# Optimization experiments

Hardware: AMD Instinct MI355X
Metric: run time of the kernel (lower is better)

The kernel has to match this reference:

```python
import jax, jax.numpy as jnp
import numpy as np

SLOPE = 25.0  # snntorch fast_sigmoid default surrogate slope

@jax.custom_vjp
def spike(u):
    return (u > 0).astype(u.dtype)

def _spike_fwd(u):
    return spike(u), u

def _spike_bwd(u, g):
    return (g / (1.0 + SLOPE * jnp.abs(u)) ** 2,)

spike.defvjp(_spike_fwd, _spike_bwd)

def fake_quant(W):
    # brevitas-style int8 per-tensor symmetric fake-quant with STE
    s = jnp.max(jnp.abs(W)) / 127.0
    q = jnp.clip(jnp.round(W / s), -127.0, 127.0) * s
    return W + jax.lax.stop_gradient(q - W)

def setup_inputs() -> dict:
    key = jax.random.key(0)
    ks = jax.random.split(key, 8)
    B, NIN, T = 256, 512, 256
    H1, H2, OUT = 512, 512, 128
    data = jax.random.normal(ks[0], (B, NIN, T), dtype=jnp.float32)
    W1 = jax.random.normal(ks[1], (H1, NIN), dtype=jnp.float32) / np.sqrt(NIN)
    W2 = jax.random.normal(ks[2], (H2, H1), dtype=jnp.float32) / np.sqrt(H1)
    Wrec = jax.random.normal(ks[3], (H2, H2), dtype=jnp.float32) / np.sqrt(H2)
    W3 = jax.random.normal(ks[4], (OUT, H2), dtype=jnp.float32) / np.sqrt(H2)
    beta = jnp.float32(0.9)
    th = jnp.float32(1.0)
    return {"data": data, "W1": W1, "W2": W2, "Wrec": Wrec, "W3": W3,
            "beta1": beta, "th1": th, "beta_r": beta, "th_r": th,
            "beta2": beta, "th2": th}

def reference(data, W1, W2, Wrec, W3, beta1, th1, beta_r, th_r, beta2, th2):
    B = data.shape[0]
    H1, H2, OUT = W1.shape[0], W2.shape[0], W3.shape[0]
    W1q = fake_quant(W1)
    W2q = fake_quant(W2)
    Wrq = fake_quant(Wrec)
    W3q = fake_quant(W3)
    b1 = jnp.clip(beta1, 0.0, 1.0)
    br = jnp.clip(beta_r, 0.0, 1.0)
    b2 = jnp.clip(beta2, 0.0, 1.0)
    # time-major input: [T, B, NIN]
    xs = jnp.transpose(data, (2, 0, 1))

    def step(carry, x):
        m1, mr, sr, m2 = carry
        # leaky1: reset zero, reset_delay=False
        m1 = b1 * m1 + x @ W1q.T
        s1 = spike(m1 - th1)
        m1 = m1 * (1.0 - s1)
        # recurrent LIF (RLeaky-like), reset zero, reset_delay=True:
        # previous spike resets the membrane at the start of this step
        h = s1 @ W2q.T + sr @ Wrq.T
        mr = (br * mr + h) * (1.0 - sr)
        sr = spike(mr - th_r)
        # leaky2: reset zero, reset_delay=False
        m2 = b2 * m2 + sr @ W3q.T
        s2 = spike(m2 - th2)
        m2 = m2 * (1.0 - s2)
        return (m1, mr, sr, m2), s2

    init = (jnp.zeros((B, H1), jnp.float32),
            jnp.zeros((B, H2), jnp.float32),
            jnp.zeros((B, H2), jnp.float32),
            jnp.zeros((B, OUT), jnp.float32))
    _, spk_rec = jax.lax.scan(step, init, xs)
    return spk_rec  # [T, B, OUT]
```

## Files before the change

### kernel.cpp

```cpp
#include <hip/hip_runtime.h>

#define B_   256
#define NIN_ 512
#define T_   256
#define H1_  512
#define H2_  512
#define OUT_ 128

typedef __attribute__((ext_vector_type(4))) int i32x4;
typedef __attribute__((address_space(1))) const unsigned int* gl_cu;
typedef __attribute__((address_space(3))) unsigned int* ls_u;

__global__ void absmax_k(const float* __restrict__ W1, const float* __restrict__ W2,
                         const float* __restrict__ Wr, const float* __restrict__ W3,
                         float* __restrict__ scales) {
  const float* W; int n;
  switch (blockIdx.x) {
    case 0:  W = W1; n = H1_ * NIN_; break;
    case 1:  W = W2; n = H2_ * H1_;  break;
    case 2:  W = Wr; n = H2_ * H2_;  break;
    default: W = W3; n = OUT_ * H2_; break;
  }
  int tid = threadIdx.x;
  float m = 0.f;
  const float4* W4 = (const float4*)W;
  int n4 = n >> 2;
  for (int i = tid; i < n4; i += 256) {
    float4 v = W4[i];
    m = fmaxf(m, fmaxf(fmaxf(fabsf(v.x), fabsf(v.y)), fmaxf(fabsf(v.z), fabsf(v.w))));
  }
  __shared__ float red[256];
  red[tid] = m;
  __syncthreads();
  for (int s = 128; s > 0; s >>= 1) {
    if (tid < s) red[tid] = fmaxf(red[tid], red[tid + s]);
    __syncthreads();
  }
  if (tid == 0) scales[blockIdx.x] = red[0] / 127.0f;
}

__global__ void quant_all_k(const float* __restrict__ W1, const float* __restrict__ W2,
                            const float* __restrict__ Wr, const float* __restrict__ W3,
                            const float* __restrict__ scales,
                            float* __restrict__ W1qT, signed char* __restrict__ W2i8,
                            signed char* __restrict__ WrT, signed char* __restrict__ W3i8) {
  const int blk = blockIdx.x;
  if (blk < 1024) {
    int idx = blk * 256 + threadIdx.x;
    int h = idx & (H1_ - 1), i = idx >> 9;
    float s = scales[0];
    float q = rintf(W1[h * NIN_ + i] / s);
    q = fminf(fmaxf(q, -127.f), 127.f);
    W1qT[idx] = q * s;
  } else if (blk < 2048) {
    int idx = (blk - 1024) * 256 + threadIdx.x;
    float s = scales[1];
    float q = rintf(W2[idx] / s);
    q = fminf(fmaxf(q, -127.f), 127.f);
    W2i8[idx] = (signed char)q;
  } else if (blk < 3072) {
    int idx = (blk - 2048) * 256 + threadIdx.x;
    int r = idx >> 9, c = idx & (H2_ - 1);
    float s = scales[2];
    float q = rintf(Wr[idx] / s);
    q = fminf(fmaxf(q, -127.f), 127.f);
    WrT[(size_t)c * H2_ + r] = (signed char)q;
  } else {
    int idx = (blk - 3072) * 256 + threadIdx.x;
    float s = scales[3];
    float q = rintf(W3[idx] / s);
    q = fminf(fmaxf(q, -127.f), 127.f);
    W3i8[idx] = (signed char)q;
  }
}

__global__ __launch_bounds__(512, 6) void gemm_cur1_k(const float* __restrict__ data,
                                                      const float* __restrict__ W1qT,
                                                      float* __restrict__ cur1) {
  const int b  = blockIdx.y;
  const int t0 = (blockIdx.x >> 2) << 7;
  const int h0 = (blockIdx.x & 3) << 7;
  const int tid = threadIdx.x;

  __shared__ float As[2][16][128];
  __shared__ float Bs[2][16][128];

  const int ty = tid >> 4, tx = tid & 15;
  const int wv = tid >> 6;
  const int ln = tid & 63;

  float acc[4][8];
#pragma unroll
  for (int i = 0; i < 4; i++)
#pragma unroll
    for (int j = 0; j < 8; j++) acc[i][j] = 0.f;

  const float* dbase = data + (size_t)b * NIN_ * T_;

  auto issue = [&](int kb, int buf) {
    const int kr = (wv << 1) + (ln >> 5);
    const float* ga = dbase + (size_t)(kb + kr) * T_ + t0 + ((ln & 31) << 2);
    __builtin_amdgcn_global_load_lds((gl_cu)ga, (ls_u)&As[buf][wv << 1][0], 16, 0, 0);
    const float* gb = W1qT + (size_t)(kb + kr) * H1_ + h0 + ((ln & 31) << 2);
    __builtin_amdgcn_global_load_lds((gl_cu)gb, (ls_u)&Bs[buf][wv << 1][0], 16, 0, 0);
  };

  issue(0, 0);

  for (int p = 0; p < 32; p++) {
    const int cur = p & 1;
    __syncthreads();
    if (p < 31) issue((p + 1) << 4, cur ^ 1);
#pragma unroll
    for (int k = 0; k < 16; k++) {
      float4 A0 = *(const float4*)&As[cur][k][ty * 4];
      float4 B0 = *(const float4*)&Bs[cur][k][tx * 4];
      float4 B1 = *(const float4*)&Bs[cur][k][64 + tx * 4];
      float a[4] = {A0.x, A0.y, A0.z, A0.w};
      float w[8] = {B0.x, B0.y, B0.z, B0.w, B1.x, B1.y, B1.z, B1.w};
#pragma unroll
      for (int i = 0; i < 4; i++)
#pragma unroll
        for (int j = 0; j < 8; j++)
          acc[i][j] = fmaf(a[i], w[j], acc[i][j]);
    }
  }

#pragma unroll
  for (int i = 0; i < 4; i++) {
    int row = ty * 4 + i;
    float* op = cur1 + (size_t)(t0 + row) * (B_ * H1_) + (size_t)b * H1_ + h0;
    float4 cA = {acc[i][0], acc[i][1], acc[i][2], acc[i][3]};
    float4 cB = {acc[i][4], acc[i][5], acc[i][6], acc[i][7]};
    *(float4*)(op + tx * 4)      = cA;
    *(float4*)(op + 64 + tx * 4) = cB;
  }
}

__global__ __launch_bounds__(256) void scan1_k(const float* __restrict__ cur1,
                                               unsigned char* __restrict__ s1u,
                                               const float* __restrict__ beta1p,
                                               const float* __restrict__ th1p) {
  const int n0 = (blockIdx.x * 256 + threadIdx.x) << 2;
  const float b1 = fminf(fmaxf(beta1p[0], 0.f), 1.f);
  const float th1 = th1p[0];
  const size_t S = (size_t)B_ * H1_;
  float m0 = 0.f, m1 = 0.f, m2 = 0.f, m3 = 0.f;
#pragma unroll 2
  for (int t = 0; t < T_; t++) {
    float4 c = *(const float4*)(cur1 + (size_t)t * S + n0);
    uchar4 o;
    m0 = b1 * m0 + c.x; bool s0 = m0 - th1 > 0.f; if (s0) m0 = 0.f; o.x = s0;
    m1 = b1 * m1 + c.y; bool s1 = m1 - th1 > 0.f; if (s1) m1 = 0.f; o.y = s1;
    m2 = b1 * m2 + c.z; bool s2 = m2 - th1 > 0.f; if (s2) m2 = 0.f; o.z = s2;
    m3 = b1 * m3 + c.w; bool s3 = m3 - th1 > 0.f; if (s3) m3 = 0.f; o.w = s3;
    *(uchar4*)(s1u + (size_t)t * S + n0) = o;
  }
}

__global__ __launch_bounds__(256) void gemm_spk_k(const unsigned char* __restrict__ A8,
                                                  const signed char* __restrict__ Bw,
                                                  float* __restrict__ C, int N) {
  __shared__ __align__(16) signed char As[128 * 80];
  __shared__ __align__(16) signed char Bs[128 * 80];
  const int tid = threadIdx.x;
  const int m0 = blockIdx.y << 7;
  const int n0 = blockIdx.x << 7;
  const int lane = tid & 63, wave = tid >> 6;
  const int quad = lane >> 4, lm = lane & 15;
  const int wm = wave << 5;

  i32x4 acc[2][8];
#pragma unroll
  for (int s = 0; s < 2; s++)
#pragma unroll
    for (int n = 0; n < 8; n++) acc[s][n] = (i32x4){0, 0, 0, 0};

  const int row = tid >> 2;
  const int offB = (tid & 3) << 4;

  for (int kb = 0; kb < 512; kb += 64) {
    uint4 av[2], bv[2];
#pragma unroll
    for (int i = 0; i < 2; i++) {
      const int r = row + (i << 6);
      av[i] = *(const uint4*)(A8 + (size_t)(m0 + r) * 512 + kb + offB);
      bv[i] = *(const uint4*)(Bw + (size_t)(n0 + r) * 512 + kb + offB);
    }
    __syncthreads();
#pragma unroll
    for (int i = 0; i < 2; i++) {
      const int r = row + (i << 6);
      *(uint4*)&As[r * 80 + offB] = av[i];
      *(uint4*)&Bs[r * 80 + offB] = bv[i];
    }
    __syncthreads();
    i32x4 a0 = *(const i32x4*)&As[(wm + lm) * 80 + (quad << 4)];
    i32x4 a1 = *(const i32x4*)&As[(wm + 16 + lm) * 80 + (quad << 4)];
    i32x4 bq[8];
#pragma unroll
    for (int n = 0; n < 8; n++)
      bq[n] = *(const i32x4*)&Bs[((n << 4) + lm) * 80 + (quad << 4)];
#pragma unroll
    for (int n = 0; n < 8; n++) {
      acc[0][n] = __builtin_amdgcn_mfma_i32_16x16x64_i8(a0, bq[n], acc[0][n], 0, 0, 0);
      acc[1][n] = __builtin_amdgcn_mfma_i32_16x16x64_i8(a1, bq[n], acc[1][n], 0, 0, 0);
    }
    __syncthreads();
  }

#pragma unroll
  for (int s = 0; s < 2; s++)
#pragma unroll
    for (int n = 0; n < 8; n++) {
      int orow = m0 + wm + (s << 4) + quad * 4;
      int col = n0 + (n << 4) + lm;
#pragma unroll
      for (int r = 0; r < 4; r++)
        C[(size_t)(orow + r) * N + col] = (float)acc[s][n][r];
    }
}

__device__ __forceinline__ void unp_add(unsigned w, int* a) {
  int iw = (int)w;
  a[0] += (iw << 24) >> 24;
  a[1] += (iw << 16) >> 24;
  a[2] += (iw << 8) >> 24;
  a[3] += iw >> 24;
}

__global__ __launch_bounds__(1024) void recurrent_k(
    const float* __restrict__ cur2a,
    const signed char* __restrict__ WrT,
    unsigned char* __restrict__ sru,
    const float* __restrict__ scales,
    const float* __restrict__ betarp, const float* __restrict__ thrp) {
  const int b = blockIdx.x;
  const int tid = threadIdx.x;
  const float s2sc = scales[1];
  const float srsc = scales[2];
  const float br = fminf(fmaxf(betarp[0], 0.f), 1.f);
  const float thr = thrp[0];

  const unsigned* WrT4 = (const unsigned*)WrT;

  __shared__ unsigned WrL[256 * 128];
  __shared__ int red[8][H2_];
  __shared__ int lstLo[2][256];
  __shared__ int lstHi[2][256];
  __shared__ int ncLo[2], ncHi[2];

  {
    const uint4* src = (const uint4*)WrT4;
    uint4* dst = (uint4*)WrL;
    for (int i = tid; i < 8192; i += 1024) dst[i] = src[i];
  }
  if (tid < 2) { ncLo[tid] = 0; ncHi[tid] = 0; }
  __syncthreads();

  float mr = 0.f, sr_own = 0.f;
  const int g = tid >> 7;
  const int c = tid & 127;

  for (int t = 0; t < T_; t++) {
    const int old = t & 1, nxt = old ^ 1;
    float c2 = 0.f;
    if (tid < H2_) c2 = cur2a[((size_t)t * B_ + b) * H2_ + tid];
    if (tid == 1022) ncLo[nxt] = 0;
    if (tid == 1023) ncHi[nxt] = 0;
    const int nLo = ncLo[old];
    const int nHi = ncHi[old];
    const int* LLo = lstLo[old];
    const int* LHi = lstHi[old];

    int a4[4] = {0, 0, 0, 0};
    {
      int k = g;
      for (; k + 56 < nLo; k += 64) {
        int i0 = LLo[k],      i1 = LLo[k + 8],  i2 = LLo[k + 16], i3 = LLo[k + 24];
        int i4 = LLo[k + 32], i5 = LLo[k + 40], i6 = LLo[k + 48], i7 = LLo[k + 56];
        unsigned w0 = WrL[(i0 << 7) + c], w1 = WrL[(i1 << 7) + c];
        unsigned w2 = WrL[(i2 << 7) + c], w3 = WrL[(i3 << 7) + c];
        unsigned w4 = WrL[(i4 << 7) + c], w5 = WrL[(i5 << 7) + c];
        unsigned w6 = WrL[(i6 << 7) + c], w7 = WrL[(i7 << 7) + c];
        unp_add(w0, a4); unp_add(w1, a4); unp_add(w2, a4); unp_add(w3, a4);
        unp_add(w4, a4); unp_add(w5, a4); unp_add(w6, a4); unp_add(w7, a4);
      }
      for (; k + 24 < nLo; k += 32) {
        int i0 = LLo[k], i1 = LLo[k + 8], i2 = LLo[k + 16], i3 = LLo[k + 24];
        unsigned w0 = WrL[(i0 << 7) + c], w1 = WrL[(i1 << 7) + c];
        unsigned w2 = WrL[(i2 << 7) + c], w3 = WrL[(i3 << 7) + c];
        unp_add(w0, a4); unp_add(w1, a4); unp_add(w2, a4); unp_add(w3, a4);
      }
      for (; k < nLo; k += 8) unp_add(WrL[(LLo[k] << 7) + c], a4);
    }
    {
      int k = g;
      for (; k + 56 < nHi; k += 64) {
        int i0 = LHi[k],      i1 = LHi[k + 8],  i2 = LHi[k + 16], i3 = LHi[k + 24];
        int i4 = LHi[k + 32], i5 = LHi[k + 40], i6 = LHi[k + 48], i7 = LHi[k + 56];
        unsigned w0 = WrT4[(i0 << 7) + c], w1 = WrT4[(i1 << 7) + c];
        unsigned w2 = WrT4[(i2 << 7) + c], w3 = WrT4[(i3 << 7) + c];
        unsigned w4 = WrT4[(i4 << 7) + c], w5 = WrT4[(i5 << 7) + c];
        unsigned w6 = WrT4[(i6 << 7) + c], w7 = WrT4[(i7 << 7) + c];
        unp_add(w0, a4); unp_add(w1, a4); unp_add(w2, a4); unp_add(w3, a4);
        unp_add(w4, a4); unp_add(w5, a4); unp_add(w6, a4); unp_add(w7, a4);
      }
      for (; k + 24 < nHi; k += 32) {
        int i0 = LHi[k], i1 = LHi[k + 8], i2 = LHi[k + 16], i3 = LHi[k + 24];
        unsigned w0 = WrT4[(i0 << 7) + c], w1 = WrT4[(i1 << 7) + c];
        unsigned w2 = WrT4[(i2 << 7) + c], w3 = WrT4[(i3 << 7) + c];
        unp_add(w0, a4); unp_add(w1, a4); unp_add(w2, a4); unp_add(w3, a4);
      }
      for (; k < nHi; k += 8) unp_add(WrT4[(LHi[k] << 7) + c], a4);
    }
    *(int4*)&red[g][c << 2] = make_int4(a4[0], a4[1], a4[2], a4[3]);
    __syncthreads();

    bool spike = false;
    if (tid < H2_) {
      int acc = red[0][tid] + red[1][tid] + red[2][tid] + red[3][tid]
              + red[4][tid] + red[5][tid] + red[6][tid] + red[7][tid];
      float h = s2sc * c2 + srsc * (float)acc;
      mr = (br * mr + h) * (1.f - sr_own);
      sr_own = (mr - thr > 0.f) ? 1.f : 0.f;
      sru[((size_t)t * B_ + b) * H2_ + tid] = (unsigned char)(sr_own != 0.f);
      spike = (sr_own != 0.f);
    }
    unsigned long long bm = __ballot(spike);
    if (bm != 0ull) {
      const int lane = tid & 63;
      const int ldr = (int)__ffsll((long long)bm) - 1;
      int* cnt = (tid < 256) ? &ncLo[nxt] : &ncHi[nxt];
      int* dst = (tid < 256) ? lstLo[nxt] : lstHi[nxt];
      int base = 0;
      if (lane == ldr) base = atomicAdd(cnt, (int)__popcll(bm));
      base = __shfl(base, ldr);
      if (spike)
        dst[base + (int)__popcll(bm & ((1ull << lane) - 1ull))] = tid;
    }
    __syncthreads();
  }
}

__global__ __launch_bounds__(256) void scan3_k(const float* __restrict__ cur3,
                                               float* __restrict__ out,
                                               const float* __restrict__ scales,
                                               const float* __restrict__ beta2p,
                                               const float* __restrict__ th2p) {
  const int n = blockIdx.x * 256 + threadIdx.x;
  const float s3sc = scales[3];
  const float b2 = fminf(fmaxf(beta2p[0], 0.f), 1.f);
  const float th2 = th2p[0];
  const size_t S = (size_t)B_ * OUT_;
  float m2 = 0.f;
  for (int t = 0; t < T_; t += 4) {
    float v0 = cur3[(size_t)t * S + n];
    float v1 = cur3[(size_t)(t + 1) * S + n];
    float v2 = cur3[(size_t)(t + 2) * S + n];
    float v3 = cur3[(size_t)(t + 3) * S + n];
    m2 = b2 * m2 + s3sc * v0; float p0 = (m2 - th2 > 0.f) ? 1.f : 0.f; m2 *= (1.f - p0);
    out[(size_t)t * S + n] = p0;
    m2 = b2 * m2 + s3sc * v1; float p1 = (m2 - th2 > 0.f) ? 1.f : 0.f; m2 *= (1.f - p1);
    out[(size_t)(t + 1) * S + n] = p1;
    m2 = b2 * m2 + s3sc * v2; float p2 = (m2 - th2 > 0.f) ? 1.f : 0.f; m2 *= (1.f - p2);
    out[(size_t)(t + 2) * S + n] = p2;
    m2 = b2 * m2 + s3sc * v3; float p3 = (m2 - th2 > 0.f) ? 1.f : 0.f; m2 *= (1.f - p3);
    out[(size_t)(t + 3) * S + n] = p3;
  }
}

extern "C" void kernel_launch(void* const* d_in, const int* in_sizes, int n_in,
                              void* d_out, int out_size, void* d_ws, size_t ws_size,
                              hipStream_t stream) {
  const float* data  = (const float*)d_in[0];
  const float* W1    = (const float*)d_in[1];
  const float* W2    = (const float*)d_in[2];
  const float* Wr    = (const float*)d_in[3];
  const float* W3    = (const float*)d_in[4];
  const float* beta1 = (const float*)d_in[5];
  const float* th1   = (const float*)d_in[6];
  const float* betar = (const float*)d_in[7];
  const float* thr   = (const float*)d_in[8];
  const float* beta2 = (const float*)d_in[9];
  const float* th2   = (const float*)d_in[10];

  char* ws = (char*)d_ws;
  float*         scales = (float*)ws;
  float*         W1qT   = (float*)(ws + 4096);
  signed char*   W2i8   = (signed char*)(ws + 4096 + 1048576);
  signed char*   W3i8   = (signed char*)(ws + 4096 + 1048576 + 524288);
  signed char*   WrT    = (signed char*)(ws + 4096 + 1048576 + 524288 + 131072);
  float*         regA   = (float*)(ws + (size_t)4194304);
  unsigned char* regB   = (unsigned char*)(ws + (size_t)4194304 + 134217728);

  float* cur1  = regA;
  float* cur2a = regA;
  float* cur3  = regA;
  unsigned char* s1u = regB;
  unsigned char* sru = regB + (size_t)33554432;

  hipLaunchKernelGGL(absmax_k, dim3(4), dim3(256), 0, stream, W1, W2, Wr, W3, scales);
  hipLaunchKernelGGL(quant_all_k, dim3(3328), dim3(256), 0, stream,
                     W1, W2, Wr, W3, scales, W1qT, W2i8, WrT, W3i8);

  hipLaunchKernelGGL(gemm_cur1_k, dim3(8, 256), dim3(512), 0, stream, data, W1qT, cur1);
  hipLaunchKernelGGL(scan1_k, dim3((B_ * H1_) / 1024), dim3(256), 0, stream, cur1, s1u, beta1, th1);
  hipLaunchKernelGGL(gemm_spk_k, dim3(4, 512), dim3(256), 0, stream, s1u, W2i8, cur2a, H2_);
  hipLaunchKernelGGL(recurrent_k, dim3(256), dim3(1024), 0, stream, cur2a, WrT, sru, scales, betar, thr);
  hipLaunchKernelGGL(gemm_spk_k, dim3(1, 512), dim3(256), 0, stream, sru, W3i8, cur3, OUT_);
  hipLaunchKernelGGL(scan3_k, dim3((B_ * OUT_) / 256), dim3(256), 0, stream, cur3, (float*)d_out, scales, beta2, th2);
}
```

Measured before the change: 1.083 ms.

## Double-buffer LDS in spike GEMM and widen scan1 parallelism to one neuron per thread

The spike GEMM now keeps two LDS buffers and issues the next K-tile's global loads before the current tile's MFMAs. This overlaps memory latency with compute and drops one barrier per iteration. The first scan kernel changes from four neurons per thread to one, launching four times as many blocks for more memory-level parallelism. The catch is scalar byte stores and 4-byte loads in place of vectorized float4/uchar4 accesses, plus twice the LDS per GEMM block, which may lower occupancy.

Result: faster. 1.035 ms (-4.4%).

```diff
diff --git a/kernel.cpp b/kernel.cpp
--- a/kernel.cpp
+++ b/kernel.cpp
@@ -141,28 +141,32 @@
                                                unsigned char* __restrict__ s1u,
                                                const float* __restrict__ beta1p,
                                                const float* __restrict__ th1p) {
-  const int n0 = (blockIdx.x * 256 + threadIdx.x) << 2;
+  const int n = blockIdx.x * 256 + threadIdx.x;
   const float b1 = fminf(fmaxf(beta1p[0], 0.f), 1.f);
   const float th1 = th1p[0];
   const size_t S = (size_t)B_ * H1_;
-  float m0 = 0.f, m1 = 0.f, m2 = 0.f, m3 = 0.f;
-#pragma unroll 2
-  for (int t = 0; t < T_; t++) {
-    float4 c = *(const float4*)(cur1 + (size_t)t * S + n0);
-    uchar4 o;
-    m0 = b1 * m0 + c.x; bool s0 = m0 - th1 > 0.f; if (s0) m0 = 0.f; o.x = s0;
-    m1 = b1 * m1 + c.y; bool s1 = m1 - th1 > 0.f; if (s1) m1 = 0.f; o.y = s1;
-    m2 = b1 * m2 + c.z; bool s2 = m2 - th1 > 0.f; if (s2) m2 = 0.f; o.z = s2;
-    m3 = b1 * m3 + c.w; bool s3 = m3 - th1 > 0.f; if (s3) m3 = 0.f; o.w = s3;
-    *(uchar4*)(s1u + (size_t)t * S + n0) = o;
+  float m1 = 0.f;
+  for (int t = 0; t < T_; t += 4) {
+    float c0 = cur1[(size_t)t * S + n];
+    float c1 = cur1[(size_t)(t + 1) * S + n];
+    float c2 = cur1[(size_t)(t + 2) * S + n];
+    float c3 = cur1[(size_t)(t + 3) * S + n];
+    m1 = b1 * m1 + c0; bool s0 = m1 - th1 > 0.f; if (s0) m1 = 0.f;
+    s1u[(size_t)t * S + n] = s0;
+    m1 = b1 * m1 + c1; bool s1 = m1 - th1 > 0.f; if (s1) m1 = 0.f;
+    s1u[(size_t)(t + 1) * S + n] = s1;
+    m1 = b1 * m1 + c2; bool s2 = m1 - th1 > 0.f; if (s2) m1 = 0.f;
+    s1u[(size_t)(t + 2) * S + n] = s2;
+    m1 = b1 * m1 + c3; bool s3 = m1 - th1 > 0.f; if (s3) m1 = 0.f;
+    s1u[(size_t)(t + 3) * S + n] = s3;
   }
 }
 
 __global__ __launch_bounds__(256) void gemm_spk_k(const unsigned char* __restrict__ A8,
                                                   const signed char* __restrict__ Bw,
                                                   float* __restrict__ C, int N) {
-  __shared__ __align__(16) signed char As[128 * 80];
-  __shared__ __align__(16) signed char Bs[128 * 80];
+  __shared__ __align__(16) signed char As[2][128 * 80];
+  __shared__ __align__(16) signed char Bs[2][128 * 80];
   const int tid = threadIdx.x;
   const int m0 = blockIdx.y << 7;
   const int n0 = blockIdx.x << 7;
@@ -179,34 +183,39 @@
   const int row = tid >> 2;
   const int offB = (tid & 3) << 4;
 
-  for (int kb = 0; kb < 512; kb += 64) {
-    uint4 av[2], bv[2];
+  uint4 av[2], bv[2];
+  auto gload = [&](int kb) {
 #pragma unroll
     for (int i = 0; i < 2; i++) {
       const int r = row + (i << 6);
       av[i] = *(const uint4*)(A8 + (size_t)(m0 + r) * 512 + kb + offB);
       bv[i] = *(const uint4*)(Bw + (size_t)(n0 + r) * 512 + kb + offB);
     }
-    __syncthreads();
+  };
+
+  gload(0);
+  int buf = 0;
+  for (int kb8 = 0; kb8 < 8; kb8++) {
 #pragma unroll
     for (int i = 0; i < 2; i++) {
       const int r = row + (i << 6);
-      *(uint4*)&As[r * 80 + offB] = av[i];
-      *(uint4*)&Bs[r * 80 + offB] = bv[i];
+      *(uint4*)&As[buf][r * 80 + offB] = av[i];
+      *(uint4*)&Bs[buf][r * 80 + offB] = bv[i];
     }
     __syncthreads();
-    i32x4 a0 = *(const i32x4*)&As[(wm + lm) * 80 + (quad << 4)];
-    i32x4 a1 = *(const i32x4*)&As[(wm + 16 + lm) * 80 + (quad << 4)];
+    if (kb8 < 7) gload((kb8 + 1) << 6);
+    i32x4 a0 = *(const i32x4*)&As[buf][(wm + lm) * 80 + (quad << 4)];
+    i32x4 a1 = *(const i32x4*)&As[buf][(wm + 16 + lm) * 80 + (quad << 4)];
     i32x4 bq[8];
 #pragma unroll
     for (int n = 0; n < 8; n++)
-      bq[n] = *(const i32x4*)&Bs[((n << 4) + lm) * 80 + (quad << 4)];
+      bq[n] = *(const i32x4*)&Bs[buf][((n << 4) + lm) * 80 + (quad << 4)];
 #pragma unroll
     for (int n = 0; n < 8; n++) {
       acc[0][n] = __builtin_amdgcn_mfma_i32_16x16x64_i8(a0, bq[n], acc[0][n], 0, 0, 0);
       acc[1][n] = __builtin_amdgcn_mfma_i32_16x16x64_i8(a1, bq[n], acc[1][n], 0, 0, 0);
     }
-    __syncthreads();
+    buf ^= 1;
   }
 
 #pragma unroll
@@ -405,7 +414,7 @@
                      W1, W2, Wr, W3, scales, W1qT, W2i8, WrT, W3i8);
 
   hipLaunchKernelGGL(gemm_cur1_k, dim3(8, 256), dim3(512), 0, stream, data, W1qT, cur1);
-  hipLaunchKernelGGL(scan1_k, dim3((B_ * H1_) / 1024), dim3(256), 0, stream, cur1, s1u, beta1, th1);
+  hipLaunchKernelGGL(scan1_k, dim3((B_ * H1_) / 256), dim3(256), 0, stream, cur1, s1u, beta1, th1);
   hipLaunchKernelGGL(gemm_spk_k, dim3(4, 512), dim3(256), 0, stream, s1u, W2i8, cur2a, H2_);
   hipLaunchKernelGGL(recurrent_k, dim3(256), dim3(1024), 0, stream, cur2a, WrT, sru, scales, betar, thr);
   hipLaunchKernelGGL(gemm_spk_k, dim3(1, 512), dim3(256), 0, stream, sru, W3i8, cur3, OUT_);
```
